# Kernel tuning notes

Measured on AMD Instinct MI355X. Metric: run time of the kernel, lower is better.

## Reference

```python
import jax, jax.numpy as jnp
import numpy as np

N_NODES = 40000
N_EDGES = 640000
IN_CH = 11
HID = 128
OUT_CH = 1
NUM_LEVELS = 2


def _lin(x, w, b):
    # torch nn.Linear: w is [out, in]
    return x @ w.T + b


def _conv(x, src, dst, w1, b1, w2, b2, w3, b3):
    # Reconstructed MLMPNNConv forward: embed, then NUM_LEVELS rounds of
    # scatter-add message passing (message = x_j), concat levels, project.
    h = jax.nn.relu(_lin(x, w1, b1))  # [N, HID]
    outs = []
    for _ in range(NUM_LEVELS):
        agg = jax.ops.segment_sum(h[src], dst, num_segments=N_NODES)  # gather + scatter-add
        h = jax.nn.relu(_lin(agg, w2, b2))
        outs.append(h)
    return _lin(jnp.concatenate(outs, axis=-1), w3, b3)  # [N, out]


def setup_inputs() -> dict:
    key = jax.random.key(0)
    ks = jax.random.split(key, 16)
    d = {}
    d["x"] = jax.random.normal(ks[0], (N_NODES, IN_CH), dtype=jnp.float32)
    d["edge_index"] = jax.random.randint(ks[1], (2, N_EDGES), 0, N_NODES, dtype=jnp.int32)
    s = 0.05
    # conv 0: lin1 IN->HID, lin2 HID->HID, lin3 2*HID->HID
    d["c0_w1"] = jax.random.normal(ks[2], (HID, IN_CH)) * s
    d["c0_b1"] = jnp.zeros((HID,), jnp.float32)
    d["c0_w2"] = jax.random.normal(ks[3], (HID, HID)) * s
    d["c0_b2"] = jnp.zeros((HID,), jnp.float32)
    d["c0_w3"] = jax.random.normal(ks[4], (HID, HID * NUM_LEVELS)) * s
    d["c0_b3"] = jnp.zeros((HID,), jnp.float32)
    # conv 1: lin1 HID->HID
    d["c1_w1"] = jax.random.normal(ks[5], (HID, HID)) * s
    d["c1_b1"] = jnp.zeros((HID,), jnp.float32)
    d["c1_w2"] = jax.random.normal(ks[6], (HID, HID)) * s
    d["c1_b2"] = jnp.zeros((HID,), jnp.float32)
    d["c1_w3"] = jax.random.normal(ks[7], (HID, HID * NUM_LEVELS)) * s
    d["c1_b3"] = jnp.zeros((HID,), jnp.float32)
    # head
    d["f_w1"] = jax.random.normal(ks[8], (HID, HID)) * s
    d["f_b1"] = jnp.zeros((HID,), jnp.float32)
    d["f_w2"] = jax.random.normal(ks[9], (OUT_CH, HID)) * s
    d["f_b2"] = jnp.zeros((OUT_CH,), jnp.float32)
    return d


def reference(x, edge_index,
              c0_w1, c0_b1, c0_w2, c0_b2, c0_w3, c0_b3,
              c1_w1, c1_b1, c1_w2, c1_b2, c1_w3, c1_b3,
              f_w1, f_b1, f_w2, f_b2):
    src, dst = edge_index[0], edge_index[1]
    h = _conv(x, src, dst, c0_w1, c0_b1, c0_w2, c0_b2, c0_w3, c0_b3)
    h = _conv(h, src, dst, c1_w1, c1_b1, c1_w2, c1_b2, c1_w3, c1_b3)
    h = jax.nn.relu(_lin(h, f_w1, f_b1))
    return _lin(h, f_w2, f_b2)  # [N, 1]
```

## Files before the change

### kernel.cpp

```cpp
#include <hip/hip_runtime.h>
#include <hip/hip_fp16.h>

#define NN 40000
#define NE 640000
#define HID 128
#define SCAN_BLK ((NN + 255) / 256)
#define EB ((NE + 255) / 256)

typedef __attribute__((ext_vector_type(8)))  short short8;
typedef __attribute__((ext_vector_type(4)))  short short4v;
typedef __attribute__((ext_vector_type(16))) float floatx16;
typedef unsigned int uint;

__device__ __forceinline__ short f2bf(float f) {
    union { float f; unsigned u; } c; c.f = f;
    unsigned u = c.u;
    unsigned r = (u + 0x7FFF + ((u >> 16) & 1)) >> 16;
    return (short)r;
}
__device__ __forceinline__ float bf2f(short h) {
    union { unsigned u; float f; } c;
    c.u = ((unsigned)(unsigned short)h) << 16;
    return c.f;
}
__device__ __forceinline__ float2 h2f2(uint u) {
    union { uint u; __half2 h; } c; c.u = u;
    return __half22float2(c.h);
}
__device__ __forceinline__ void splits(float f, short* hi, short* lo) {
    short h = f2bf(f);
    *hi = h;
    *lo = f2bf(f - bf2f(h));
}
__device__ __forceinline__ void unpack8(uint4 a, uint4 b, short8* h, short8* l) {
    short8 H, L;
    H[0] = (short)(a.x >> 16); L[0] = (short)a.x;
    H[1] = (short)(a.y >> 16); L[1] = (short)a.y;
    H[2] = (short)(a.z >> 16); L[2] = (short)a.z;
    H[3] = (short)(a.w >> 16); L[3] = (short)a.w;
    H[4] = (short)(b.x >> 16); L[4] = (short)b.x;
    H[5] = (short)(b.y >> 16); L[5] = (short)b.y;
    H[6] = (short)(b.z >> 16); L[6] = (short)b.z;
    H[7] = (short)(b.w >> 16); L[7] = (short)b.w;
    *h = H; *l = L;
}

__device__ __forceinline__ int wswz(int o, int k) {
    int chunk = k >> 4, half = (k >> 3) & 1, j = k & 7;
    int ct = o >> 5, m31 = o & 31;
    int lane = half * 32 + m31;
    return (((chunk * 4 + ct) * 64 + lane) * 8 + j);
}

#define ACCH(u, A)                                      \
    { float2 f0 = h2f2(u.x), f1 = h2f2(u.y);            \
      A.x += f0.x; A.y += f0.y; A.z += f1.x; A.w += f1.y; }

__global__ __launch_bounds__(256, 4) void fused_gather_lin_kernel(
    const __half* __restrict__ h, const int* __restrict__ row_ptr,
    const int* __restrict__ esrc, const uint* __restrict__ Wq,
    const float* __restrict__ bias, __half* __restrict__ out)
{
    __shared__ short sAh[4096];
    __shared__ short sAl[4096];
    __shared__ int   sCtr;
    const int t  = threadIdx.x;
    const int r0 = blockIdx.x * 32;
    const int c4 = t & 31;
    const int sub = c4 >> 1;
    const int j0  = (c4 & 1) * 4;
    const uint2* hp = (const uint2*)h;

    if (t == 0) sCtr = 0;
    __syncthreads();

    for (;;) {
        int n = 0;
        if ((t & 31) == 0) n = atomicAdd(&sCtr, 1);
        n = __shfl(n, 0, 32);
        if (n >= 32) break;
        const int node = r0 + n;
        const int lo = row_ptr[node], hi = row_ptr[node + 1];
        float4 a = make_float4(0,0,0,0), b = make_float4(0,0,0,0);
        float4 c = make_float4(0,0,0,0), d = make_float4(0,0,0,0);
        int e = lo;
        for (; e + 8 <= hi; e += 8) {
            int s0 = esrc[e],   s1 = esrc[e+1], s2 = esrc[e+2], s3 = esrc[e+3];
            int s4 = esrc[e+4], s5 = esrc[e+5], s6 = esrc[e+6], s7 = esrc[e+7];
            uint2 u0 = hp[(size_t)s0 * 32 + c4];
            uint2 u1 = hp[(size_t)s1 * 32 + c4];
            uint2 u2 = hp[(size_t)s2 * 32 + c4];
            uint2 u3 = hp[(size_t)s3 * 32 + c4];
            uint2 u4 = hp[(size_t)s4 * 32 + c4];
            uint2 u5 = hp[(size_t)s5 * 32 + c4];
            uint2 u6 = hp[(size_t)s6 * 32 + c4];
            uint2 u7 = hp[(size_t)s7 * 32 + c4];
            ACCH(u0, a); ACCH(u1, b); ACCH(u2, c); ACCH(u3, d);
            ACCH(u4, a); ACCH(u5, b); ACCH(u6, c); ACCH(u7, d);
        }
        for (; e + 4 <= hi; e += 4) {
            int s0 = esrc[e], s1 = esrc[e+1], s2 = esrc[e+2], s3 = esrc[e+3];
            uint2 u0 = hp[(size_t)s0 * 32 + c4];
            uint2 u1 = hp[(size_t)s1 * 32 + c4];
            uint2 u2 = hp[(size_t)s2 * 32 + c4];
            uint2 u3 = hp[(size_t)s3 * 32 + c4];
            ACCH(u0, a); ACCH(u1, b); ACCH(u2, c); ACCH(u3, d);
        }
        for (; e < hi; ++e) {
            int s0 = esrc[e];
            uint2 u0 = hp[(size_t)s0 * 32 + c4];
            ACCH(u0, a);
        }
        float vx = (a.x + b.x) + (c.x + d.x);
        float vy = (a.y + b.y) + (c.y + d.y);
        float vz = (a.z + b.z) + (c.z + d.z);
        float vw = (a.w + b.w) + (c.w + d.w);
        short4v Hq, Lq;
        short hh, ll;
        splits(vx, &hh, &ll); Hq.x = hh; Lq.x = ll;
        splits(vy, &hh, &ll); Hq.y = hh; Lq.y = ll;
        splits(vz, &hh, &ll); Hq.z = hh; Lq.z = ll;
        splits(vw, &hh, &ll); Hq.w = hh; Lq.w = ll;
        const int off = sub * 256 + n * 8 + j0;
        *(short4v*)(sAh + off) = Hq;
        *(short4v*)(sAl + off) = Lq;
    }
    __syncthreads();

    const int wv   = t >> 6;
    const int lane = t & 63;
    const int m31  = lane & 31;
    const int half = lane >> 5;
    floatx16 acc;
    #pragma unroll
    for (int i = 0; i < 16; ++i) acc[i] = 0.f;
    #pragma unroll
    for (int c = 0; c < 8; ++c) {
        short8 ah = *(const short8*)(sAh + (c * 2 + half) * 256 + m31 * 8);
        short8 al = *(const short8*)(sAl + (c * 2 + half) * 256 + m31 * 8);
        const uint* wr = Wq + ((size_t)(c * 4 + wv) * 64 + lane) * 8;
        uint4 w0 = *(const uint4*)(wr);
        uint4 w1 = *(const uint4*)(wr + 4);
        short8 bh, bl;
        unpack8(w0, w1, &bh, &bl);
        acc = __builtin_amdgcn_mfma_f32_32x32x16_bf16(ah, bh, acc, 0, 0, 0);
        acc = __builtin_amdgcn_mfma_f32_32x32x16_bf16(al, bh, acc, 0, 0, 0);
        acc = __builtin_amdgcn_mfma_f32_32x32x16_bf16(ah, bl, acc, 0, 0, 0);
    }
    const int col = wv * 32 + m31;
    const float bb = bias[col];
    #pragma unroll
    for (int reg = 0; reg < 16; ++reg) {
        int row = (reg & 3) + 8 * (reg >> 2) + 4 * half;
        float v = fmaxf(acc[reg] + bb, 0.f);
        out[(size_t)(r0 + row) * HID + col] = __float2half(v);
    }
}

template<int PHASES, bool RELU>
__global__ __launch_bounds__(256, 4) void lin32_kernel(
    const __half* __restrict__ X0, const __half* __restrict__ X1,
    const uint* __restrict__ Wq, const float* __restrict__ bias,
    __half* __restrict__ out)
{
    __shared__ short sAh[PHASES * 4096];
    __shared__ short sAl[PHASES * 4096];
    const int t  = threadIdx.x;
    const int r0 = blockIdx.x * 32;

    #pragma unroll
    for (int i = 0; i < PHASES * 4; ++i) {
        int v = t + 256 * i;
        const __half* Xp = (PHASES == 2 && v >= 1024) ? X1 : X0;
        int vv  = v & 1023;
        int row = vv >> 5, q = vv & 31;
        uint2 u = *(const uint2*)(Xp + (size_t)(r0 + row) * 128 + q * 4);
        float2 f0 = h2f2(u.x), f1 = h2f2(u.y);
        int kk  = ((PHASES == 2) ? (v >> 10) * 128 : 0) + q * 4;
        int off = (kk >> 3) * 256 + row * 8 + (q & 1) * 4;
        short4v hi, lo;
        short hh, ll;
        splits(f0.x, &hh, &ll); hi.x = hh; lo.x = ll;
        splits(f0.y, &hh, &ll); hi.y = hh; lo.y = ll;
        splits(f1.x, &hh, &ll); hi.z = hh; lo.z = ll;
        splits(f1.y, &hh, &ll); hi.w = hh; lo.w = ll;
        *(short4v*)(sAh + off) = hi;
        *(short4v*)(sAl + off) = lo;
    }
    __syncthreads();

    const int wv   = t >> 6;
    const int lane = t & 63;
    const int m31  = lane & 31;
    const int half = lane >> 5;
    floatx16 acc;
    #pragma unroll
    for (int i = 0; i < 16; ++i) acc[i] = 0.f;
    #pragma unroll
    for (int c = 0; c < PHASES * 8; ++c) {
        short8 ah = *(const short8*)(sAh + (c * 2 + half) * 256 + m31 * 8);
        short8 al = *(const short8*)(sAl + (c * 2 + half) * 256 + m31 * 8);
        const uint* wr = Wq + ((size_t)(c * 4 + wv) * 64 + lane) * 8;
        uint4 w0 = *(const uint4*)(wr);
        uint4 w1 = *(const uint4*)(wr + 4);
        short8 bh, bl;
        unpack8(w0, w1, &bh, &bl);
        acc = __builtin_amdgcn_mfma_f32_32x32x16_bf16(ah, bh, acc, 0, 0, 0);
        acc = __builtin_amdgcn_mfma_f32_32x32x16_bf16(al, bh, acc, 0, 0, 0);
        acc = __builtin_amdgcn_mfma_f32_32x32x16_bf16(ah, bl, acc, 0, 0, 0);
    }
    const int col = wv * 32 + m31;
    const float bb = bias[col];
    #pragma unroll
    for (int reg = 0; reg < 16; ++reg) {
        int row = (reg & 3) + 8 * (reg >> 2) + 4 * half;
        float v = acc[reg] + bb;
        if (RELU) v = fmaxf(v, 0.f);
        out[(size_t)(r0 + row) * HID + col] = __float2half(v);
    }
}

__global__ __launch_bounds__(256, 3) void cat_head_kernel(
    const __half* __restrict__ X0, const __half* __restrict__ X1,
    const uint* __restrict__ Wq, const float* __restrict__ bias,
    const float* __restrict__ f2, const float* __restrict__ f2b,
    float* __restrict__ out)
{
    __shared__ short sAh[8192];
    __shared__ short sAl[8192];
    __shared__ float gbuf[32 * 129];
    const int t  = threadIdx.x;
    const int r0 = blockIdx.x * 32;

    #pragma unroll
    for (int i = 0; i < 8; ++i) {
        int v = t + 256 * i;
        const __half* Xp = (v >= 1024) ? X1 : X0;
        int vv  = v & 1023;
        int row = vv >> 5, q = vv & 31;
        uint2 u = *(const uint2*)(Xp + (size_t)(r0 + row) * 128 + q * 4);
        float2 f0 = h2f2(u.x), f1 = h2f2(u.y);
        int kk  = (v >> 10) * 128 + q * 4;
        int off = (kk >> 3) * 256 + row * 8 + (q & 1) * 4;
        short4v hi, lo;
        short hh, ll;
        splits(f0.x, &hh, &ll); hi.x = hh; lo.x = ll;
        splits(f0.y, &hh, &ll); hi.y = hh; lo.y = ll;
        splits(f1.x, &hh, &ll); hi.z = hh; lo.z = ll;
        splits(f1.y, &hh, &ll); hi.w = hh; lo.w = ll;
        *(short4v*)(sAh + off) = hi;
        *(short4v*)(sAl + off) = lo;
    }
    __syncthreads();

    const int wv   = t >> 6;
    const int lane = t & 63;
    const int m31  = lane & 31;
    const int half = lane >> 5;
    floatx16 acc;
    #pragma unroll
    for (int i = 0; i < 16; ++i) acc[i] = 0.f;
    #pragma unroll
    for (int c = 0; c < 16; ++c) {
        short8 ah = *(const short8*)(sAh + (c * 2 + half) * 256 + m31 * 8);
        short8 al = *(const short8*)(sAl + (c * 2 + half) * 256 + m31 * 8);
        const uint* wr = Wq + ((size_t)(c * 4 + wv) * 64 + lane) * 8;
        uint4 w0 = *(const uint4*)(wr);
        uint4 w1 = *(const uint4*)(wr + 4);
        short8 bh, bl;
        unpack8(w0, w1, &bh, &bl);
        acc = __builtin_amdgcn_mfma_f32_32x32x16_bf16(ah, bh, acc, 0, 0, 0);
        acc = __builtin_amdgcn_mfma_f32_32x32x16_bf16(al, bh, acc, 0, 0, 0);
        acc = __builtin_amdgcn_mfma_f32_32x32x16_bf16(ah, bl, acc, 0, 0, 0);
    }
    const int col = wv * 32 + m31;
    const float bb = bias[col];
    #pragma unroll
    for (int reg = 0; reg < 16; ++reg) {
        int row = (reg & 3) + 8 * (reg >> 2) + 4 * half;
        gbuf[row * 129 + col] = fmaxf(acc[reg] + bb, 0.f);
    }
    __syncthreads();

    const int node = t >> 3;
    const int seg  = t & 7;
    const float* gr = gbuf + node * 129 + seg * 16;
    float a = 0.f;
    #pragma unroll
    for (int i = 0; i < 16; ++i) a += gr[i] * f2[seg * 16 + i];
    a += __shfl_down(a, 4, 8);
    a += __shfl_down(a, 2, 8);
    a += __shfl_down(a, 1, 8);
    if (seg == 0) out[r0 + node] = a + f2b[0];
}

__global__ __launch_bounds__(256) void prep_kernel(
    const float* __restrict__ c0w2, const float* __restrict__ c1w2,
    const float* __restrict__ c1w1, const float* __restrict__ c0w3,
    const float* __restrict__ c0b3, const float* __restrict__ c1b1,
    const float* __restrict__ fw1,  const float* __restrict__ c1w3,
    const float* __restrict__ c1b3, const float* __restrict__ fb1,
    const int* __restrict__ dst, int* __restrict__ cnt,
    uint* __restrict__ wp, uint* __restrict__ p_Wa, uint* __restrict__ p_Wb,
    float* __restrict__ f_ba, float* __restrict__ f_bb)
{
    const int b = blockIdx.x;
    const int t = threadIdx.x;
    if (b < 128) {
        int i = b * 256 + t;
        const float* src = (i < 16384) ? c0w2 : c1w2;
        int off = (i < 16384) ? 0 : 16384;
        int L = i - off;
        int o = L >> 7, k = L & 127;
        short hh, ll;
        splits(src[L], &hh, &ll);
        wp[off + wswz(o, k)] = ((uint)(unsigned short)hh << 16) | (uint)(unsigned short)ll;
    } else if (b < 384) {
        const bool isA = (b < 256);
        const int o = b - (isA ? 128 : 256);
        const float* A   = isA ? c1w1 : fw1;
        const float* B   = isA ? c0w3 : c1w3;
        const float* bi  = isA ? c0b3 : c1b3;
        const float* bo  = isA ? c1b1 : fb1;
        uint*  W  = isA ? p_Wa : p_Wb;
        float* bb = isA ? f_ba : f_bb;
        const float* Ar = A + o * 128;
        float s = 0.f;
        for (int j = 0; j < 128; ++j) s += Ar[j] * B[j * 256 + t];
        short hh, ll;
        splits(s, &hh, &ll);
        W[wswz(o, t)] = ((uint)(unsigned short)hh << 16) | (uint)(unsigned short)ll;
        if (t == 0) {
            float sb = 0.f;
            for (int j = 0; j < 128; ++j) sb += Ar[j] * bi[j];
            bb[o] = sb + bo[o];
        }
    } else {
        int e = (b - 384) * 256 + t;
        if (e < NE) atomicAdd(&cnt[dst[e]], 1);
    }
}

__global__ __launch_bounds__(256) void scan1_kernel(
    const int* __restrict__ cnt, int* __restrict__ row_ptr,
    int* __restrict__ partials)
{
    __shared__ int s[256];
    const int t = threadIdx.x;
    const int i = blockIdx.x * 256 + t;
    int v = (i < NN) ? cnt[i] : 0;
    s[t] = v;
    __syncthreads();
    #pragma unroll
    for (int off = 1; off < 256; off <<= 1) {
        int x = (t >= off) ? s[t - off] : 0;
        __syncthreads();
        s[t] += x;
        __syncthreads();
    }
    if (i < NN) row_ptr[i] = s[t] - v;
    if (t == 255) partials[blockIdx.x] = s[255];
}

__global__ __launch_bounds__(256) void scan2_kernel(
    int* __restrict__ partials, int* __restrict__ row_ptr)
{
    __shared__ int s[256];
    const int t = threadIdx.x;
    int v = (t < SCAN_BLK) ? partials[t] : 0;
    s[t] = v;
    __syncthreads();
    #pragma unroll
    for (int off = 1; off < 256; off <<= 1) {
        int x = (t >= off) ? s[t - off] : 0;
        __syncthreads();
        s[t] += x;
        __syncthreads();
    }
    if (t < SCAN_BLK) partials[t] = s[t] - v;
    if (t == 255) row_ptr[NN] = s[255];
}

__global__ __launch_bounds__(256) void scan3_kernel(
    int* __restrict__ row_ptr, const int* __restrict__ partials)
{
    const int i = blockIdx.x * 256 + threadIdx.x;
    if (i < NN) row_ptr[i] += partials[blockIdx.x];
}

__global__ __launch_bounds__(256) void fill_embed_kernel(
    const int* __restrict__ src, const int* __restrict__ dst,
    const int* __restrict__ row_ptr, int* __restrict__ pos,
    int* __restrict__ esrc,
    const float* __restrict__ x, const float* __restrict__ w1,
    const float* __restrict__ b1, __half* __restrict__ h0)
{
    const int b = blockIdx.x;
    const int t = threadIdx.x;
    if (b < EB) {
        int e = b * 256 + t;
        if (e < NE) {
            int d = dst[e];
            int p = row_ptr[d] + atomicAdd(&pos[d], 1);
            esrc[p] = src[e];
        }
    } else {
        __shared__ float xs[2][88];
        const int hf = t >> 7;
        const int m  = t & 127;
        const int r0 = (b - EB) * 16 + hf * 8;
        for (int i = m; i < 88; i += 128) {
            int r = i / 11, k = i - r * 11;
            xs[hf][i] = x[(size_t)(r0 + r) * 11 + k];
        }
        __syncthreads();
        float acc[8] = {};
        const float* Wm = w1 + m * 11;
        #pragma unroll
        for (int k = 0; k < 11; ++k) {
            float w = Wm[k];
            #pragma unroll
            for (int r = 0; r < 8; ++r) acc[r] += xs[hf][r * 11 + k] * w;
        }
        const float bias = b1[m];
        #pragma unroll
        for (int r = 0; r < 8; ++r) {
            float v = fmaxf(acc[r] + bias, 0.f);
            h0[(size_t)(r0 + r) * HID + m] = __float2half(v);
        }
    }
}

extern "C" void kernel_launch(void* const* d_in, const int* in_sizes, int n_in,
                              void* d_out, int out_size, void* d_ws, size_t ws_size,
                              hipStream_t stream)
{
    const float* x     = (const float*)d_in[0];
    const int*   eidx  = (const int*)d_in[1];
    const float* c0_w1 = (const float*)d_in[2],  *c0_b1 = (const float*)d_in[3];
    const float* c0_w2 = (const float*)d_in[4],  *c0_b2 = (const float*)d_in[5];
    const float* c0_w3 = (const float*)d_in[6],  *c0_b3 = (const float*)d_in[7];
    const float* c1_w1 = (const float*)d_in[8],  *c1_b1 = (const float*)d_in[9];
    const float* c1_w2 = (const float*)d_in[10], *c1_b2 = (const float*)d_in[11];
    const float* c1_w3 = (const float*)d_in[12], *c1_b3 = (const float*)d_in[13];
    const float* f_w1  = (const float*)d_in[14], *f_b1  = (const float*)d_in[15];
    const float* f_w2  = (const float*)d_in[16], *f_b2  = (const float*)d_in[17];
    const int* src = eidx;
    const int* dst = eidx + NE;
    float* out = (float*)d_out;

    const size_t BUF = (size_t)NN * HID;
    __half* bA = (__half*)d_ws;
    __half* bB = bA + BUF;
    __half* bC = bB + BUF;
    int* row_ptr  = (int*)(bC + BUF);
    int* cnt      = row_ptr + (NN + 1);
    int* pos      = cnt + NN;
    int* esrc     = pos + NN;
    int* partials = esrc + NE;
    uint* wp      = (uint*)(partials + SCAN_BLK);

    uint* p_c0w2 = wp + 0;
    uint* p_c1w2 = wp + 16384;
    uint* p_Wa   = wp + 32768;
    uint* p_Wb   = wp + 65536;
    float* f_ba  = (float*)(wp + 98304);
    float* f_bb  = f_ba + 128;

    const int nbl = (NN + 31) / 32;

    (void)hipMemsetAsync(cnt, 0, 2 * NN * sizeof(int), stream);
    prep_kernel<<<384 + EB, 256, 0, stream>>>(
        c0_w2, c1_w2, c1_w1, c0_w3, c0_b3, c1_b1,
        f_w1, c1_w3, c1_b3, f_b1, dst, cnt, wp, p_Wa, p_Wb, f_ba, f_bb);
    scan1_kernel<<<SCAN_BLK, 256, 0, stream>>>(cnt, row_ptr, partials);
    scan2_kernel<<<1, 256, 0, stream>>>(partials, row_ptr);
    scan3_kernel<<<SCAN_BLK, 256, 0, stream>>>(row_ptr, partials);
    fill_embed_kernel<<<EB + 2500, 256, 0, stream>>>(
        src, dst, row_ptr, pos, esrc, x, c0_w1, c0_b1, bA);

    fused_gather_lin_kernel<<<nbl, 256, 0, stream>>>(bA, row_ptr, esrc, p_c0w2, c0_b2, bB);
    fused_gather_lin_kernel<<<nbl, 256, 0, stream>>>(bB, row_ptr, esrc, p_c0w2, c0_b2, bC);
    lin32_kernel<2, true><<<nbl, 256, 0, stream>>>(bB, bC, p_Wa, f_ba, bA);

    fused_gather_lin_kernel<<<nbl, 256, 0, stream>>>(bA, row_ptr, esrc, p_c1w2, c1_b2, bB);
    fused_gather_lin_kernel<<<nbl, 256, 0, stream>>>(bB, row_ptr, esrc, p_c1w2, c1_b2, bC);
    cat_head_kernel<<<nbl, 256, 0, stream>>>(bB, bC, p_Wb, f_bb, f_w2, f_b2, out);
}
```

Baseline: 319.2 us.

## Stage block edge lists in LDS and gather rows with 16-byte loads

Each block now stages its 33 row pointers and up to 1536 source indices into shared memory before gathering, with a fallback to global reads when a block has more edges. The gather switches from 8-byte loads by 32 lanes to 16-byte loads by 16 lanes, with two half-warps each taking alternate edges and combining their partial sums through a shuffle. The aim is fewer, wider memory transactions and no repeated global index loads, at the cost of extra LDS, one more barrier, and a cross-lane reduction per node.

```diff
diff --git a/kernel.cpp b/kernel.cpp
--- a/kernel.cpp
+++ b/kernel.cpp
@@ -6,6 +6,7 @@
 #define HID 128
 #define SCAN_BLK ((NN + 255) / 256)
 #define EB ((NE + 255) / 256)
+#define ECAP 1536
 
 typedef __attribute__((ext_vector_type(8)))  short short8;
 typedef __attribute__((ext_vector_type(4)))  short short4v;
@@ -52,9 +53,36 @@
     return (((chunk * 4 + ct) * 64 + lane) * 8 + j);
 }
 
-#define ACCH(u, A)                                      \
-    { float2 f0 = h2f2(u.x), f1 = h2f2(u.y);            \
-      A.x += f0.x; A.y += f0.y; A.z += f1.x; A.w += f1.y; }
+#define ACC4(u, A, B)                                                     \
+    { float2 f0 = h2f2(u.x), f1 = h2f2(u.y);                              \
+      float2 f2 = h2f2(u.z), f3 = h2f2(u.w);                              \
+      A.x += f0.x; A.y += f0.y; A.z += f1.x; A.w += f1.y;                 \
+      B.x += f2.x; B.y += f2.y; B.z += f3.x; B.w += f3.y; }
+
+#define GBODY(IDX)                                                        \
+        for (; e + 8 <= hi; e += 8) {                                     \
+            int s0 = IDX(e + sub);     int s1 = IDX(e + 2 + sub);         \
+            int s2 = IDX(e + 4 + sub); int s3 = IDX(e + 6 + sub);         \
+            uint4 u0 = hp[(size_t)s0 * 16 + c16];                         \
+            uint4 u1 = hp[(size_t)s1 * 16 + c16];                         \
+            uint4 u2 = hp[(size_t)s2 * 16 + c16];                         \
+            uint4 u3 = hp[(size_t)s3 * 16 + c16];                         \
+            ACC4(u0, a0, a1); ACC4(u1, b0, b1);                           \
+            ACC4(u2, c0, c1); ACC4(u3, d0, d1);                           \
+        }                                                                 \
+        for (; e + 2 <= hi; e += 2) {                                     \
+            int s0 = IDX(e + sub);                                        \
+            uint4 u0 = hp[(size_t)s0 * 16 + c16];                         \
+            ACC4(u0, a0, a1);                                             \
+        }                                                                 \
+        if (sub == 0 && e < hi) {                                         \
+            int s0 = IDX(e);                                              \
+            uint4 u0 = hp[(size_t)s0 * 16 + c16];                         \
+            ACC4(u0, b0, b1);                                             \
+        }
+
+#define IDXS(j) sE[(j)]
+#define IDXG(j) esrc[lo0 + (j)]
 
 __global__ __launch_bounds__(256, 4) void fused_gather_lin_kernel(
     const __half* __restrict__ h, const int* __restrict__ row_ptr,
@@ -63,67 +91,69 @@
 {
     __shared__ short sAh[4096];
     __shared__ short sAl[4096];
+    __shared__ int   sE[ECAP];
+    __shared__ int   sRP[33];
     __shared__ int   sCtr;
-    const int t  = threadIdx.x;
-    const int r0 = blockIdx.x * 32;
-    const int c4 = t & 31;
-    const int sub = c4 >> 1;
-    const int j0  = (c4 & 1) * 4;
-    const uint2* hp = (const uint2*)h;
+    const int t   = threadIdx.x;
+    const int r0  = blockIdx.x * 32;
+    const int c16 = t & 15;
+    const int sub = (t >> 4) & 1;
+    const uint4* hp = (const uint4*)h;
 
     if (t == 0) sCtr = 0;
-    __syncthreads();
+    if (t < 33) sRP[t] = row_ptr[r0 + t];
+    __syncthreads();
+    const int lo0 = sRP[0];
+    const int nE  = sRP[32] - lo0;
+    const int nStage = nE < ECAP ? nE : ECAP;
+    for (int i = t; i < nStage; i += 256) sE[i] = esrc[lo0 + i];
+    __syncthreads();
+    const bool fast = (nE <= ECAP);
 
     for (;;) {
         int n = 0;
         if ((t & 31) == 0) n = atomicAdd(&sCtr, 1);
         n = __shfl(n, 0, 32);
         if (n >= 32) break;
-        const int node = r0 + n;
-        const int lo = row_ptr[node], hi = row_ptr[node + 1];
-        float4 a = make_float4(0,0,0,0), b = make_float4(0,0,0,0);
-        float4 c = make_float4(0,0,0,0), d = make_float4(0,0,0,0);
+        const int lo = sRP[n] - lo0, hi = sRP[n + 1] - lo0;
+        float4 a0 = make_float4(0,0,0,0), a1 = make_float4(0,0,0,0);
+        float4 b0 = make_float4(0,0,0,0), b1 = make_float4(0,0,0,0);
+        float4 c0 = make_float4(0,0,0,0), c1 = make_float4(0,0,0,0);
+        float4 d0 = make_float4(0,0,0,0), d1 = make_float4(0,0,0,0);
         int e = lo;
-        for (; e + 8 <= hi; e += 8) {
-            int s0 = esrc[e],   s1 = esrc[e+1], s2 = esrc[e+2], s3 = esrc[e+3];
-            int s4 = esrc[e+4], s5 = esrc[e+5], s6 = esrc[e+6], s7 = esrc[e+7];
-            uint2 u0 = hp[(size_t)s0 * 32 + c4];
-            uint2 u1 = hp[(size_t)s1 * 32 + c4];
-            uint2 u2 = hp[(size_t)s2 * 32 + c4];
-            uint2 u3 = hp[(size_t)s3 * 32 + c4];
-            uint2 u4 = hp[(size_t)s4 * 32 + c4];
-            uint2 u5 = hp[(size_t)s5 * 32 + c4];
-            uint2 u6 = hp[(size_t)s6 * 32 + c4];
-            uint2 u7 = hp[(size_t)s7 * 32 + c4];
-            ACCH(u0, a); ACCH(u1, b); ACCH(u2, c); ACCH(u3, d);
-            ACCH(u4, a); ACCH(u5, b); ACCH(u6, c); ACCH(u7, d);
-        }
-        for (; e + 4 <= hi; e += 4) {
-            int s0 = esrc[e], s1 = esrc[e+1], s2 = esrc[e+2], s3 = esrc[e+3];
-            uint2 u0 = hp[(size_t)s0 * 32 + c4];
-            uint2 u1 = hp[(size_t)s1 * 32 + c4];
-            uint2 u2 = hp[(size_t)s2 * 32 + c4];
-            uint2 u3 = hp[(size_t)s3 * 32 + c4];
-            ACCH(u0, a); ACCH(u1, b); ACCH(u2, c); ACCH(u3, d);
-        }
-        for (; e < hi; ++e) {
-            int s0 = esrc[e];
-            uint2 u0 = hp[(size_t)s0 * 32 + c4];
-            ACCH(u0, a);
-        }
-        float vx = (a.x + b.x) + (c.x + d.x);
-        float vy = (a.y + b.y) + (c.y + d.y);
-        float vz = (a.z + b.z) + (c.z + d.z);
-        float vw = (a.w + b.w) + (c.w + d.w);
-        short4v Hq, Lq;
-        short hh, ll;
-        splits(vx, &hh, &ll); Hq.x = hh; Lq.x = ll;
-        splits(vy, &hh, &ll); Hq.y = hh; Lq.y = ll;
-        splits(vz, &hh, &ll); Hq.z = hh; Lq.z = ll;
-        splits(vw, &hh, &ll); Hq.w = hh; Lq.w = ll;
-        const int off = sub * 256 + n * 8 + j0;
-        *(short4v*)(sAh + off) = Hq;
-        *(short4v*)(sAl + off) = Lq;
+        if (fast) { GBODY(IDXS) } else { GBODY(IDXG) }
+        float4 v0, v1;
+        v0.x = (a0.x + b0.x) + (c0.x + d0.x);
+        v0.y = (a0.y + b0.y) + (c0.y + d0.y);
+        v0.z = (a0.z + b0.z) + (c0.z + d0.z);
+        v0.w = (a0.w + b0.w) + (c0.w + d0.w);
+        v1.x = (a1.x + b1.x) + (c1.x + d1.x);
+        v1.y = (a1.y + b1.y) + (c1.y + d1.y);
+        v1.z = (a1.z + b1.z) + (c1.z + d1.z);
+        v1.w = (a1.w + b1.w) + (c1.w + d1.w);
+        v0.x += __shfl_down(v0.x, 16, 32);
+        v0.y += __shfl_down(v0.y, 16, 32);
+        v0.z += __shfl_down(v0.z, 16, 32);
+        v0.w += __shfl_down(v0.w, 16, 32);
+        v1.x += __shfl_down(v1.x, 16, 32);
+        v1.y += __shfl_down(v1.y, 16, 32);
+        v1.z += __shfl_down(v1.z, 16, 32);
+        v1.w += __shfl_down(v1.w, 16, 32);
+        if (sub == 0) {
+            short8 H, L;
+            short hh, ll;
+            splits(v0.x, &hh, &ll); H[0] = hh; L[0] = ll;
+            splits(v0.y, &hh, &ll); H[1] = hh; L[1] = ll;
+            splits(v0.z, &hh, &ll); H[2] = hh; L[2] = ll;
+            splits(v0.w, &hh, &ll); H[3] = hh; L[3] = ll;
+            splits(v1.x, &hh, &ll); H[4] = hh; L[4] = ll;
+            splits(v1.y, &hh, &ll); H[5] = hh; L[5] = ll;
+            splits(v1.z, &hh, &ll); H[6] = hh; L[6] = ll;
+            splits(v1.w, &hh, &ll); H[7] = hh; L[7] = ll;
+            const int off = c16 * 256 + n * 8;
+            *(short8*)(sAh + off) = H;
+            *(short8*)(sAl + off) = L;
+        }
     }
     __syncthreads();
 
```

After: 306.5 us. -4.0%, faster.
